# Performance work log

Hardware: AMD Instinct MI355X
Metric: run time of the kernel (lower is better)

## Reference

```python
import jax, jax.numpy as jnp
import numpy as np

B, C, H, W = 8, 512, 64, 64
CH = C // 2          # channels per branch after chunk
R = CH // 4          # reduced channels (reduction=4)


def conv1x1(x, w, b):
    # x: [B,c,H,W], w: [o,c], b: [o]  (1x1 conv == per-pixel matmul)
    return jnp.einsum('oc,bchw->bohw', w, x) + b[None, :, None, None]


def spatial_self_corr(x, w1, b1, w2, b2, wo, bo):
    # DANet-style position attention. x: [B,CH,H,W]
    b_, c_, h_, w_ = x.shape
    n = h_ * w_
    q = conv1x1(x, w1, b1).reshape(b_, -1, n)   # [B,R,N]
    k = conv1x1(x, w2, b2).reshape(b_, -1, n)   # [B,R,N]
    attn = jax.nn.softmax(jnp.einsum('brn,brm->bnm', q, k), axis=-1)  # [B,N,N]
    out = jnp.einsum('brn,bnm->brm', k, attn)   # v = k (reduced channels), [B,R,N]
    out = out.reshape(b_, -1, h_, w_)
    return conv1x1(out, wo, bo)                 # [B,CH,H,W]


def channel_self_corr(x, wq, bq, wk, bk, wo, bo):
    # DANet-style channel attention over reduced channels. x: [B,CH,H,W]
    b_, c_, h_, w_ = x.shape
    n = h_ * w_
    q = conv1x1(x, wq, bq).reshape(b_, -1, n)   # [B,R,N]
    k = conv1x1(x, wk, bk).reshape(b_, -1, n)   # [B,R,N]
    attn = jax.nn.softmax(jnp.einsum('brn,bsn->brs', q, k), axis=-1)  # [B,R,R]
    out = jnp.einsum('brs,bsn->brn', attn, k)   # v = k (reduced channels)
    out = out.reshape(b_, -1, h_, w_)
    return conv1x1(out, wo, bo)                 # [B,CH,H,W]


def ckam_forward(top_feat, bottom_feat, wt, bt, wb, bb,
                 s_w1, s_b1, s_w2, s_b2, s_wo, s_bo,
                 c_wq, c_bq, c_wk, c_bk, c_wo, c_bo, f_w, f_b):
    top = conv1x1(top_feat, wt, bt)
    bottom = conv1x1(bottom_feat, wb, bb)
    x = top + bottom                            # [B,C,H,W]
    x1, x2 = jnp.split(x, 2, axis=1)            # each [B,C/2,H,W]
    ssc_out = spatial_self_corr(x1, s_w1, s_b1, s_w2, s_b2, s_wo, s_bo)
    csc_out = channel_self_corr(x2, c_wq, c_bq, c_wk, c_bk, c_wo, c_bo)
    out = jnp.concatenate([ssc_out, csc_out], axis=1)  # [B,C,H,W]
    return conv1x1(out, f_w, f_b)


def setup_inputs() -> dict:
    key = jax.random.key(0)
    ks = jax.random.split(key, 24)
    s = 0.02
    d = {
        'top_feat': jax.random.normal(ks[0], (B, C, H, W), jnp.float32),
        'bottom_feat': jax.random.normal(ks[1], (B, C, H, W), jnp.float32),
        'wt': jax.random.normal(ks[2], (C, C), jnp.float32) * s,
        'bt': jnp.zeros((C,), jnp.float32),
        'wb': jax.random.normal(ks[3], (C, C), jnp.float32) * s,
        'bb': jnp.zeros((C,), jnp.float32),
        's_w1': jax.random.normal(ks[4], (R, CH), jnp.float32) * s,
        's_b1': jnp.zeros((R,), jnp.float32),
        's_w2': jax.random.normal(ks[5], (R, CH), jnp.float32) * s,
        's_b2': jnp.zeros((R,), jnp.float32),
        's_wo': jax.random.normal(ks[6], (CH, R), jnp.float32) * s,
        's_bo': jnp.zeros((CH,), jnp.float32),
        'c_wq': jax.random.normal(ks[7], (R, CH), jnp.float32) * s,
        'c_bq': jnp.zeros((R,), jnp.float32),
        'c_wk': jax.random.normal(ks[8], (R, CH), jnp.float32) * s,
        'c_bk': jnp.zeros((R,), jnp.float32),
        'c_wo': jax.random.normal(ks[9], (CH, R), jnp.float32) * s,
        'c_bo': jnp.zeros((CH,), jnp.float32),
        'f_w': jax.random.normal(ks[10], (C, C), jnp.float32) * s,
        'f_b': jnp.zeros((C,), jnp.float32),
    }
    return d


def reference(top_feat, bottom_feat, wt, bt, wb, bb,
              s_w1, s_b1, s_w2, s_b2, s_wo, s_bo,
              c_wq, c_bq, c_wk, c_bk, c_wo, c_bo, f_w, f_b):
    return ckam_forward(top_feat, bottom_feat, wt, bt, wb, bb,
                        s_w1, s_b1, s_w2, s_b2, s_wo, s_bo,
                        c_wq, c_bq, c_wk, c_bk, c_wo, c_bo, f_w, f_b)
```

## Files before the change

kernel.cpp:

```cpp
#include <hip/hip_runtime.h>

typedef unsigned short u16;
typedef unsigned int   u32;
typedef __attribute__((ext_vector_type(8))) short short8;
typedef __attribute__((ext_vector_type(4))) float f32x4;

__device__ __forceinline__ u16 f2bf(float f) {
  u32 u = __float_as_uint(f);
  u32 r = u + 0x7fffu + ((u >> 16) & 1u);
  return (u16)(r >> 16);
}

__device__ __forceinline__ void gl_lds16(const u16* g, u16* l) {
  __builtin_amdgcn_global_load_lds(
      (const __attribute__((address_space(1))) u32*)g,
      (__attribute__((address_space(3))) u32*)l, 16, 0, 0);
}

__global__ __launch_bounds__(256) void k_combine_qk(
    const float* __restrict__ wt, const float* __restrict__ bt,
    const float* __restrict__ wb, const float* __restrict__ bb,
    const float* __restrict__ s_w1, const float* __restrict__ s_b1,
    const float* __restrict__ s_w2, const float* __restrict__ s_b2,
    const float* __restrict__ c_wq, const float* __restrict__ c_bq,
    const float* __restrict__ c_wk, const float* __restrict__ c_bk,
    u16* __restrict__ Wqkb, float* __restrict__ bqk) {
  int j = blockIdx.x;
  int g = j >> 6, r = j & 63;
  const float* sw; const float* sb;
  if (g == 0)      { sw = s_w1; sb = s_b1; }
  else if (g == 1) { sw = s_w2; sb = s_b2; }
  else if (g == 2) { sw = c_wq; sb = c_bq; }
  else             { sw = c_wk; sb = c_bk; }
  int cbase = (g < 2) ? 0 : 256;

  __shared__ float swr[256];
  __shared__ float red[256];
  int t = threadIdx.x;
  swr[t] = sw[r * 256 + t];
  __syncthreads();

  float a0 = 0.f, a1 = 0.f, a2 = 0.f, a3 = 0.f;
#pragma unroll 4
  for (int c = 0; c < 256; ++c) {
    float a = swr[c];
    int row = (cbase + c) * 512;
    a0 += a * wt[row + t];
    a1 += a * wt[row + 256 + t];
    a2 += a * wb[row + t];
    a3 += a * wb[row + 256 + t];
  }
  Wqkb[j * 1024 + t]       = f2bf(a0);
  Wqkb[j * 1024 + 256 + t] = f2bf(a1);
  Wqkb[j * 1024 + 512 + t] = f2bf(a2);
  Wqkb[j * 1024 + 768 + t] = f2bf(a3);

  red[t] = swr[t] * (bt[cbase + t] + bb[cbase + t]);
  __syncthreads();
  for (int s = 128; s > 0; s >>= 1) {
    if (t < s) red[t] += red[t + s];
    __syncthreads();
  }
  if (t == 0) bqk[j] = red[0] + sb[r];
}

__global__ __launch_bounds__(128) void k_combine_f(
    const float* __restrict__ f_w, const float* __restrict__ f_b,
    const float* __restrict__ s_wo, const float* __restrict__ s_bo,
    const float* __restrict__ c_wo, const float* __restrict__ c_bo,
    u16* __restrict__ Wfb, float* __restrict__ bfb) {
  int o = blockIdx.x;
  int t = threadIdx.x;
  __shared__ float fwr[512];
  __shared__ float red[128];
  for (int i = t; i < 512; i += 128) fwr[i] = f_w[o * 512 + i];
  __syncthreads();

  float acc = 0.f;
  if (t < 64) {
#pragma unroll 4
    for (int c = 0; c < 256; ++c) acc += fwr[c] * s_wo[c * 64 + t];
  } else {
    int rr = t - 64;
#pragma unroll 4
    for (int c = 0; c < 256; ++c) acc += fwr[256 + c] * c_wo[c * 64 + rr];
  }
  Wfb[o * 128 + t] = f2bf(acc);

  red[t] = fwr[t] * s_bo[t] + fwr[t + 128] * s_bo[t + 128]
         + fwr[256 + t] * c_bo[t] + fwr[384 + t] * c_bo[t + 128];
  __syncthreads();
  for (int s = 64; s > 0; s >>= 1) {
    if (t < s) red[t] += red[t + s];
    __syncthreads();
  }
  if (t == 0) bfb[o] = red[0] + f_b[o];
}

__global__ __launch_bounds__(256) void k_gemm_qk_mfma(
    const float* __restrict__ top, const float* __restrict__ bot,
    const u16* __restrict__ Wqkb, const float* __restrict__ bqk,
    float* __restrict__ qk) {
  int b = blockIdx.z, j0 = blockIdx.y * 128, n0 = blockIdx.x * 128;
  __shared__ __align__(16) u16 Aj[2][128][32];
  __shared__ __align__(16) u16 Xs[2][128][32];
  int t = threadIdx.x;
  int wv = t >> 6, lane = t & 63;
  int wr = wv >> 1, wc = wv & 1;
  int q = lane >> 4, l = lane & 15;

  f32x4 acc[4][4];
#pragma unroll
  for (int tr = 0; tr < 4; ++tr)
#pragma unroll
    for (int tc = 0; tc < 4; ++tc) acc[tr][tc] = (f32x4){0.f, 0.f, 0.f, 0.f};

  int a = t & 31;
  int xs = t >> 5;
  int asr4 = lane >> 2;
  int asc = (lane & 3) ^ ((asr4 + (asr4 >> 2)) & 3);
  int rowA = wr * 64 + l;
  int rowX = wc * 64 + l;
  int fswA = (q ^ ((rowA + (rowA >> 2)) & 3)) << 4;
  int fswX = (q ^ ((rowX + (rowX >> 2)) & 3)) << 4;

  f32x4 xva[4], xvb[4];

  auto stageA = [&](int kc, u16* dst) {
#pragma unroll
    for (int pp = 0; pp < 2; ++pp) {
      int p = wv * 2 + pp;
      int row = p * 16 + asr4;
      gl_lds16(Wqkb + (size_t)(j0 + row) * 1024 + kc + asc * 8, dst + p * 512);
    }
  };
  auto loadX = [&](int kc, f32x4 (&xv)[4]) {
    const float* src = (kc < 512) ? top : bot;
    int c0 = kc & 511;
    const float* xb = src + (size_t)(b * 512 + c0) * 4096 + n0 + 4 * a;
#pragma unroll
    for (int d = 0; d < 4; ++d)
      xv[d] = *reinterpret_cast<const f32x4*>(&xb[(size_t)(4 * xs + d) * 4096]);
  };
  auto writeX = [&](f32x4 (&xv)[4], u16* dst) {
    char* base = reinterpret_cast<char*>(dst);
#pragma unroll
    for (int i = 0; i < 4; ++i) {
      int n = 4 * a + i;
      int key = (n + (n >> 2)) & 3;
      int col = ((((xs >> 1) ^ key) << 4) | ((xs & 1) << 3));
      uint2 pk;
      pk.x = (u32)f2bf(xv[0][i]) | ((u32)f2bf(xv[1][i]) << 16);
      pk.y = (u32)f2bf(xv[2][i]) | ((u32)f2bf(xv[3][i]) << 16);
      *reinterpret_cast<uint2*>(base + n * 64 + col) = pk;
    }
  };
  auto compute = [&](int bufsel) {
    const char* Ab = reinterpret_cast<const char*>(&Aj[bufsel][0][0]);
    const char* Xb = reinterpret_cast<const char*>(&Xs[bufsel][0][0]);
    short8 af[4], bfr[4];
#pragma unroll
    for (int tr = 0; tr < 4; ++tr)
      af[tr] = *reinterpret_cast<const short8*>(Ab + (rowA + tr * 16) * 64 + fswA);
#pragma unroll
    for (int tc = 0; tc < 4; ++tc)
      bfr[tc] = *reinterpret_cast<const short8*>(Xb + (rowX + tc * 16) * 64 + fswX);
#pragma unroll
    for (int tr = 0; tr < 4; ++tr)
#pragma unroll
      for (int tc = 0; tc < 4; ++tc)
        acc[tr][tc] = __builtin_amdgcn_mfma_f32_16x16x32_bf16(
            af[tr], bfr[tc], acc[tr][tc], 0, 0, 0);
  };

  stageA(0, &Aj[0][0][0]);
  loadX(0, xva);
  writeX(xva, &Xs[0][0][0]);
  loadX(32, xvb);
  asm volatile("s_waitcnt lgkmcnt(0)" ::: "memory");
  __builtin_amdgcn_s_barrier();

  for (int it2 = 0; it2 < 15; ++it2) {
    int e = it2 * 2;
    stageA((e + 1) * 32, &Aj[1][0][0]);
    loadX((e + 2) * 32, xva);
    writeX(xvb, &Xs[1][0][0]);
    compute(0);
    asm volatile("s_waitcnt vmcnt(4) lgkmcnt(0)" ::: "memory");
    __builtin_amdgcn_s_barrier();
    stageA((e + 2) * 32, &Aj[0][0][0]);
    loadX((e + 3) * 32, xvb);
    writeX(xva, &Xs[0][0][0]);
    compute(1);
    asm volatile("s_waitcnt vmcnt(4) lgkmcnt(0)" ::: "memory");
    __builtin_amdgcn_s_barrier();
  }
  stageA(31 * 32, &Aj[1][0][0]);
  writeX(xvb, &Xs[1][0][0]);
  compute(0);
  asm volatile("s_waitcnt vmcnt(0) lgkmcnt(0)" ::: "memory");
  __builtin_amdgcn_s_barrier();
  compute(1);

#pragma unroll
  for (int tr = 0; tr < 4; ++tr) {
    int j = j0 + wr * 64 + tr * 16 + q * 4;
    float4 bias = *reinterpret_cast<const float4*>(&bqk[j]);
#pragma unroll
    for (int tc = 0; tc < 4; ++tc) {
      int n = n0 + wc * 64 + tc * 16 + l;
      float* dst = qk + (size_t)(b * 256 + j) * 4096 + n;
      dst[0]        = acc[tr][tc][0] + bias.x;
      dst[4096]     = acc[tr][tc][1] + bias.y;
      dst[2 * 4096] = acc[tr][tc][2] + bias.z;
      dst[3 * 4096] = acc[tr][tc][3] + bias.w;
    }
  }
}

__global__ __launch_bounds__(256) void k_transpose_qk(
    const float* __restrict__ qk, u16* __restrict__ q1t, u16* __restrict__ k1t) {
  int b = blockIdx.y, n0 = blockIdx.x * 64;
  int t = threadIdx.x;
  int a = t & 15;
  int c = t >> 4;
  int jb = 8 * (c & 7);
  const float* src =
      qk + ((size_t)(b * 256) + (c >> 3) * 64 + jb) * 4096 + n0 + 4 * a;
  f32x4 v[8];
#pragma unroll
  for (int i = 0; i < 8; ++i)
    v[i] = *reinterpret_cast<const f32x4*>(&src[(size_t)i * 4096]);
  u16* dstbase = (c < 8) ? q1t : k1t;
#pragma unroll
  for (int i = 0; i < 4; ++i) {
    int n = n0 + 4 * a + i;
    u32 pk[4];
#pragma unroll
    for (int kk = 0; kk < 4; ++kk)
      pk[kk] = (u32)f2bf(v[2 * kk][i]) | ((u32)f2bf(v[2 * kk + 1][i]) << 16);
    *reinterpret_cast<uint4*>(dstbase + ((size_t)(b * 4096) + n) * 64 + jb) =
        *reinterpret_cast<const uint4*>(pk);
  }
}

__global__ __launch_bounds__(256) void k_sp_stats_mfma(
    const u16* __restrict__ q1t, const u16* __restrict__ k1t,
    const float* __restrict__ qk, u16* __restrict__ k1d) {
  int b = blockIdx.y, n0 = blockIdx.x * 64;
  __shared__ u16 Qs[64][72];
  __shared__ float red[4][64][16];
  __shared__ float dvs[64];
  int t = threadIdx.x;
  int wv = t >> 6, lane = t & 63;
  int q = lane >> 4, l = lane & 15;

  {
    const u32* src = reinterpret_cast<const u32*>(q1t + ((size_t)(b * 4096) + n0) * 64);
    for (int i = t; i < 2048; i += 256) {
      int n = i >> 5, c = i & 31;
      reinterpret_cast<u32*>(&Qs[n][0])[c] = src[n * 32 + c];
    }
  }
  __syncthreads();

  short8 afr[4][2];
#pragma unroll
  for (int tn = 0; tn < 4; ++tn)
#pragma unroll
    for (int kh = 0; kh < 2; ++kh)
      afr[tn][kh] = *reinterpret_cast<const short8*>(&Qs[tn * 16 + l][kh * 32 + q * 8]);

  const u16* kbase = k1t + (size_t)b * 4096 * 64;
  float dsum[4][4];
#pragma unroll
  for (int tn = 0; tn < 4; ++tn)
#pragma unroll
    for (int i = 0; i < 4; ++i) dsum[tn][i] = 0.f;

  for (int mt = wv; mt < 64; mt += 4) {
    int m0 = mt * 64;
#pragma unroll
    for (int tm = 0; tm < 4; ++tm) {
      const u16* kp = kbase + ((size_t)(m0 + tm * 16 + l)) * 64;
      short8 b0 = *reinterpret_cast<const short8*>(kp + q * 8);
      short8 b1 = *reinterpret_cast<const short8*>(kp + 32 + q * 8);
#pragma unroll
      for (int tn = 0; tn < 4; ++tn) {
        f32x4 acc = {0.f, 0.f, 0.f, 0.f};
        acc = __builtin_amdgcn_mfma_f32_16x16x32_bf16(afr[tn][0], b0, acc, 0, 0, 0);
        acc = __builtin_amdgcn_mfma_f32_16x16x32_bf16(afr[tn][1], b1, acc, 0, 0, 0);
#pragma unroll
        for (int i = 0; i < 4; ++i) dsum[tn][i] += __expf(acc[i]);
      }
    }
  }

#pragma unroll
  for (int tn = 0; tn < 4; ++tn)
#pragma unroll
    for (int i = 0; i < 4; ++i)
      red[wv][tn * 16 + q * 4 + i][l] = dsum[tn][i];
  __syncthreads();
  if (t < 64) {
    float s = 0.f;
#pragma unroll
    for (int v = 0; v < 4; ++v)
#pragma unroll
      for (int u = 0; u < 16; ++u) s += red[v][t][u];
    dvs[t] = 1.0f / s;
  }
  __syncthreads();

  const float* k1src = qk + ((size_t)(b * 256) + 64) * 4096 + n0;
  u16* kdst = k1d + (size_t)(b * 64) * 4096 + n0;
  for (int i = t; i < 4096; i += 256) {
    int r = i >> 6, n = i & 63;
    kdst[(size_t)r * 4096 + n] = f2bf(k1src[(size_t)r * 4096 + n] * dvs[n]);
  }
}

#define NSPLIT 2

__device__ __forceinline__ void stage_qk(const u16* qb, const u16* kb, int noff,
                                         u16* qdst, u16* kdst,
                                         int wv, int rsub, int scol) {
#pragma unroll
  for (int pp = 0; pp < 2; ++pp) {
    int p = wv * 2 + pp;
    int row = p * 8 + rsub;
    gl_lds16(qb + ((size_t)(noff + row)) * 64 + scol * 8, qdst + p * 512);
    gl_lds16(kb + (size_t)row * 4096 + noff + scol * 8, kdst + p * 512);
  }
}

__global__ __launch_bounds__(256) void k_sp_apply_mfma(
    const u16* __restrict__ q1t, const u16* __restrict__ k1t,
    const u16* __restrict__ k1d, float* __restrict__ spre) {
  int b = blockIdx.z, m0 = blockIdx.x * 64;
  int n_base = blockIdx.y * (4096 / NSPLIT);
  const int NT = 64 / NSPLIT;

  __shared__ __align__(16) u16 Qs[2][64][64];
  __shared__ __align__(16) u16 Ks[2][64][64];
  __shared__ __align__(16) u16 Wt[64][64];

  int t = threadIdx.x;
  int wv = t >> 6, lane = t & 63;
  int q = lane >> 4, l = lane & 15;
  int sw = l & 7;
  int rsub = lane >> 3;
  int scol = (lane & 7) ^ rsub;

  const u16* ktp = k1t + ((size_t)(b * 4096) + m0 + wv * 16 + l) * 64;
  short8 bS0 = *reinterpret_cast<const short8*>(ktp + q * 8);
  short8 bS1 = *reinterpret_cast<const short8*>(ktp + 32 + q * 8);

  const u16* qb = q1t + (size_t)b * 4096 * 64;
  const u16* kb = k1d + (size_t)b * 64 * 4096;

  f32x4 accO[4];
#pragma unroll
  for (int tr = 0; tr < 4; ++tr) accO[tr] = (f32x4){0.f, 0.f, 0.f, 0.f};

  stage_qk(qb, kb, n_base, &Qs[0][0][0], &Ks[0][0][0], wv, rsub, scol);
  __syncthreads();

  int wrow = wv * 16 + l;
  char* wp = reinterpret_cast<char*>(&Wt[wrow][0]);
  int c_a0 = (q ^ sw) << 4;
  int c_a1 = c_a0 ^ 64;

  int cur = 0;
  for (int nt = 0; nt < NT; ++nt) {
    if (nt + 1 < NT)
      stage_qk(qb, kb, n_base + (nt + 1) * 64,
               &Qs[cur ^ 1][0][0], &Ks[cur ^ 1][0][0], wv, rsub, scol);

    const u16(*Qc)[64] = Qs[cur];
    const u16(*Kc)[64] = Ks[cur];

#pragma unroll
    for (int tn = 0; tn < 4; ++tn) {
      const char* qrow = reinterpret_cast<const char*>(&Qc[tn * 16 + l][0]);
      short8 a0 = *reinterpret_cast<const short8*>(qrow + c_a0);
      short8 a1 = *reinterpret_cast<const short8*>(qrow + c_a1);
      f32x4 s = {0.f, 0.f, 0.f, 0.f};
      s = __builtin_amdgcn_mfma_f32_16x16x32_bf16(a0, bS0, s, 0, 0, 0);
      s = __builtin_amdgcn_mfma_f32_16x16x32_bf16(a1, bS1, s, 0, 0, 0);
      u16 w0 = f2bf(__expf(s[0]));
      u16 w1 = f2bf(__expf(s[1]));
      u16 w2 = f2bf(__expf(s[2]));
      u16 w3 = f2bf(__expf(s[3]));
      uint2 pk;
      pk.x = (u32)w0 | ((u32)w1 << 16);
      pk.y = (u32)w2 | ((u32)w3 << 16);
      *reinterpret_cast<uint2*>(
          wp + ((((tn * 2 + (q >> 1)) ^ sw) << 4) | ((q & 1) << 3))) = pk;
    }

    short8 bW0 = *reinterpret_cast<const short8*>(wp + c_a0);
    short8 bW1 = *reinterpret_cast<const short8*>(wp + c_a1);
#pragma unroll
    for (int tr = 0; tr < 4; ++tr) {
      const char* krow = reinterpret_cast<const char*>(&Kc[tr * 16 + l][0]);
      short8 a0 = *reinterpret_cast<const short8*>(krow + c_a0);
      short8 a1 = *reinterpret_cast<const short8*>(krow + c_a1);
      accO[tr] = __builtin_amdgcn_mfma_f32_16x16x32_bf16(a0, bW0, accO[tr], 0, 0, 0);
      accO[tr] = __builtin_amdgcn_mfma_f32_16x16x32_bf16(a1, bW1, accO[tr], 0, 0, 0);
    }

    __syncthreads();
    cur ^= 1;
  }

#pragma unroll
  for (int tr = 0; tr < 4; ++tr)
#pragma unroll
    for (int i = 0; i < 4; ++i)
      atomicAdd(&spre[(size_t)(b * 64 + tr * 16 + q * 4 + i) * 4096 + m0 + wrow],
                accO[tr][i]);
}

__global__ __launch_bounds__(256) void k_ch_scores(
    const float* __restrict__ qk, float* __restrict__ part) {
  int b = blockIdx.y, ch = blockIdx.x;
  const float* q2 = qk + (size_t)(b * 256 + 128) * 4096;
  const float* k2 = qk + (size_t)(b * 256 + 192) * 4096;
  __shared__ float Qs[64][65];
  __shared__ float Ks[64][65];
  int t = threadIdx.x, ti = t >> 4, tj = t & 15;
  float acc[4][4] = {};

  for (int sub = 0; sub < 2; ++sub) {
    int n0 = ch * 128 + sub * 64;
    __syncthreads();
    for (int i = t; i < 4096; i += 256) {
      int r = i >> 6, n = i & 63;
      Qs[r][n] = q2[(size_t)r * 4096 + n0 + n];
      Ks[r][n] = k2[(size_t)r * 4096 + n0 + n];
    }
    __syncthreads();
#pragma unroll
    for (int n = 0; n < 64; ++n) {
      float qa[4], ka[4];
#pragma unroll
      for (int i = 0; i < 4; ++i) qa[i] = Qs[ti * 4 + i][n];
#pragma unroll
      for (int jx = 0; jx < 4; ++jx) ka[jx] = Ks[tj * 4 + jx][n];
#pragma unroll
      for (int i = 0; i < 4; ++i)
#pragma unroll
        for (int jx = 0; jx < 4; ++jx) acc[i][jx] += qa[i] * ka[jx];
    }
  }
#pragma unroll
  for (int i = 0; i < 4; ++i)
#pragma unroll
    for (int jx = 0; jx < 4; ++jx)
      part[(size_t)(b * 32 + ch) * 4096 + (ti * 4 + i) * 64 + tj * 4 + jx] = acc[i][jx];
}

__global__ __launch_bounds__(64) void k_ch_softmax(
    const float* __restrict__ part, float* __restrict__ attn2) {
  int bid = blockIdx.x;
  int b = bid >> 6, r = bid & 63;
  int s = threadIdx.x;
  const float* p0 = part + (size_t)(b * 32) * 4096 + r * 64 + s;
  float sum = 0.f;
#pragma unroll
  for (int c = 0; c < 32; ++c) sum += p0[(size_t)c * 4096];
  float mx = sum;
#pragma unroll
  for (int o = 32; o > 0; o >>= 1) mx = fmaxf(mx, __shfl_xor(mx, o));
  float e = __expf(sum - mx);
  float den = e;
#pragma unroll
  for (int o = 32; o > 0; o >>= 1) den += __shfl_xor(den, o);
  attn2[(size_t)b * 4096 + r * 64 + s] = e / den;
}

__global__ __launch_bounds__(256) void k_ch_apply(
    const float* __restrict__ qk, const float* __restrict__ attn2,
    float* __restrict__ cpre) {
  int b = blockIdx.y;
  int t = threadIdx.x;
  int n = blockIdx.x * 64 + (t & 63);
  int qr = t >> 6;
  const float* k2 = qk + (size_t)(b * 256 + 192) * 4096;
  __shared__ float As[64][64];
  {
    float4* As4 = reinterpret_cast<float4*>(&As[0][0]);
    const float4* a4 = reinterpret_cast<const float4*>(attn2 + (size_t)b * 4096);
    for (int i = t; i < 1024; i += 256) As4[i] = a4[i];
  }
  __syncthreads();

  float acc[16];
#pragma unroll
  for (int rr = 0; rr < 16; ++rr) acc[rr] = 0.f;
  for (int s4 = 0; s4 < 64; s4 += 4) {
    float kv0 = k2[(size_t)(s4 + 0) * 4096 + n];
    float kv1 = k2[(size_t)(s4 + 1) * 4096 + n];
    float kv2 = k2[(size_t)(s4 + 2) * 4096 + n];
    float kv3 = k2[(size_t)(s4 + 3) * 4096 + n];
#pragma unroll
    for (int rr = 0; rr < 16; ++rr) {
      float4 w = *reinterpret_cast<const float4*>(&As[qr * 16 + rr][s4]);
      acc[rr] += w.x * kv0 + w.y * kv1 + w.z * kv2 + w.w * kv3;
    }
  }
#pragma unroll
  for (int rr = 0; rr < 16; ++rr)
    cpre[(size_t)(b * 64 + qr * 16 + rr) * 4096 + n] = acc[rr];
}

__global__ __launch_bounds__(256) void k_final_mfma(
    const float* __restrict__ spre, const float* __restrict__ cpre,
    const u16* __restrict__ Wfb, const float* __restrict__ bfb,
    float* __restrict__ out) {
  int b = blockIdx.z, o0 = blockIdx.y * 128, n0 = blockIdx.x * 128;
  __shared__ __align__(16) u16 Aj[2][128][32];
  __shared__ __align__(16) u16 Xs[2][128][32];
  int t = threadIdx.x;
  int wv = t >> 6, lane = t & 63;
  int wr = wv >> 1, wc = wv & 1;
  int q = lane >> 4, l = lane & 15;

  f32x4 acc[4][4];
#pragma unroll
  for (int tr = 0; tr < 4; ++tr)
#pragma unroll
    for (int tc = 0; tc < 4; ++tc) acc[tr][tc] = (f32x4){0.f, 0.f, 0.f, 0.f};

  int a = t & 31;
  int xs = t >> 5;
  int asr4 = lane >> 2;
  int asc = (lane & 3) ^ ((asr4 + (asr4 >> 2)) & 3);
  int rowA = wr * 64 + l;
  int rowX = wc * 64 + l;
  int fswA = (q ^ ((rowA + (rowA >> 2)) & 3)) << 4;
  int fswX = (q ^ ((rowX + (rowX >> 2)) & 3)) << 4;

  f32x4 xva[4], xvb[4];

  auto stageA = [&](int kc, u16* dst) {
#pragma unroll
    for (int pp = 0; pp < 2; ++pp) {
      int p = wv * 2 + pp;
      int row = p * 16 + asr4;
      gl_lds16(Wfb + (size_t)(o0 + row) * 128 + kc + asc * 8, dst + p * 512);
    }
  };
  auto loadX = [&](int kc, f32x4 (&xv)[4]) {
    const float* src = (kc < 64) ? spre : cpre;
    int r0 = kc & 63;
    const float* xb = src + (size_t)(b * 64 + r0) * 4096 + n0 + 4 * a;
#pragma unroll
    for (int d = 0; d < 4; ++d)
      xv[d] = *reinterpret_cast<const f32x4*>(&xb[(size_t)(4 * xs + d) * 4096]);
  };
  auto writeX = [&](f32x4 (&xv)[4], u16* dst) {
    char* base = reinterpret_cast<char*>(dst);
#pragma unroll
    for (int i = 0; i < 4; ++i) {
      int n = 4 * a + i;
      int key = (n + (n >> 2)) & 3;
      int col = ((((xs >> 1) ^ key) << 4) | ((xs & 1) << 3));
      uint2 pk;
      pk.x = (u32)f2bf(xv[0][i]) | ((u32)f2bf(xv[1][i]) << 16);
      pk.y = (u32)f2bf(xv[2][i]) | ((u32)f2bf(xv[3][i]) << 16);
      *reinterpret_cast<uint2*>(base + n * 64 + col) = pk;
    }
  };
  auto compute = [&](int bufsel) {
    const char* Ab = reinterpret_cast<const char*>(&Aj[bufsel][0][0]);
    const char* Xb = reinterpret_cast<const char*>(&Xs[bufsel][0][0]);
    short8 af[4], bfr[4];
#pragma unroll
    for (int tr = 0; tr < 4; ++tr)
      af[tr] = *reinterpret_cast<const short8*>(Ab + (rowA + tr * 16) * 64 + fswA);
#pragma unroll
    for (int tc = 0; tc < 4; ++tc)
      bfr[tc] = *reinterpret_cast<const short8*>(Xb + (rowX + tc * 16) * 64 + fswX);
#pragma unroll
    for (int tr = 0; tr < 4; ++tr)
#pragma unroll
      for (int tc = 0; tc < 4; ++tc)
        acc[tr][tc] = __builtin_amdgcn_mfma_f32_16x16x32_bf16(
            af[tr], bfr[tc], acc[tr][tc], 0, 0, 0);
  };

  stageA(0, &Aj[0][0][0]);
  loadX(0, xva);
  writeX(xva, &Xs[0][0][0]);
  loadX(32, xvb);
  asm volatile("s_waitcnt lgkmcnt(0)" ::: "memory");
  __builtin_amdgcn_s_barrier();
  stageA(32, &Aj[1][0][0]);
  loadX(64, xva);
  writeX(xvb, &Xs[1][0][0]);
  compute(0);
  asm volatile("s_waitcnt vmcnt(4) lgkmcnt(0)" ::: "memory");
  __builtin_amdgcn_s_barrier();
  stageA(64, &Aj[0][0][0]);
  loadX(96, xvb);
  writeX(xva, &Xs[0][0][0]);
  compute(1);
  asm volatile("s_waitcnt vmcnt(4) lgkmcnt(0)" ::: "memory");
  __builtin_amdgcn_s_barrier();
  stageA(96, &Aj[1][0][0]);
  writeX(xvb, &Xs[1][0][0]);
  compute(0);
  asm volatile("s_waitcnt vmcnt(0) lgkmcnt(0)" ::: "memory");
  __builtin_amdgcn_s_barrier();
  compute(1);

#pragma unroll
  for (int tr = 0; tr < 4; ++tr) {
    int o = o0 + wr * 64 + tr * 16 + q * 4;
    float4 bias = *reinterpret_cast<const float4*>(&bfb[o]);
#pragma unroll
    for (int tc = 0; tc < 4; ++tc) {
      int n = n0 + wc * 64 + tc * 16 + l;
      float* dst = out + (size_t)(b * 512 + o) * 4096 + n;
      dst[0]        = acc[tr][tc][0] + bias.x;
      dst[4096]     = acc[tr][tc][1] + bias.y;
      dst[2 * 4096] = acc[tr][tc][2] + bias.z;
      dst[3 * 4096] = acc[tr][tc][3] + bias.w;
    }
  }
}

extern "C" void kernel_launch(void* const* d_in, const int* in_sizes, int n_in,
                              void* d_out, int out_size, void* d_ws, size_t ws_size,
                              hipStream_t stream) {
  const float* top  = (const float*)d_in[0];
  const float* bot  = (const float*)d_in[1];
  const float* wt   = (const float*)d_in[2];
  const float* bt   = (const float*)d_in[3];
  const float* wb   = (const float*)d_in[4];
  const float* bb   = (const float*)d_in[5];
  const float* s_w1 = (const float*)d_in[6];
  const float* s_b1 = (const float*)d_in[7];
  const float* s_w2 = (const float*)d_in[8];
  const float* s_b2 = (const float*)d_in[9];
  const float* s_wo = (const float*)d_in[10];
  const float* s_bo = (const float*)d_in[11];
  const float* c_wq = (const float*)d_in[12];
  const float* c_bq = (const float*)d_in[13];
  const float* c_wk = (const float*)d_in[14];
  const float* c_bk = (const float*)d_in[15];
  const float* c_wo = (const float*)d_in[16];
  const float* c_bo = (const float*)d_in[17];
  const float* f_w  = (const float*)d_in[18];
  const float* f_b  = (const float*)d_in[19];
  float* out = (float*)d_out;

  char* ob = (char*)d_out;
  float* qk = (float*)ob;
  u16* q1t = (u16*)(ob + 33554432);
  u16* k1t = (u16*)(ob + 37748736);
  u16* k1d = (u16*)(ob + 41943040);
  float* part = (float*)(ob + 46137344);

  char* ws = (char*)d_ws;
  float* attn2 = (float*)(ws + 1179648);
  float* spre  = (float*)(ws + 1310720);
  float* cpre  = (float*)(ws + 9699328);
  u16*   Wqkb  = (u16*)  (ws + 18087936);
  float* bqk   = (float*)(ws + 18612224);
  u16*   Wfb   = (u16*)  (ws + 18613248);
  float* bfb   = (float*)(ws + 18744320);

  hipMemsetAsync(spre, 0, 8388608, stream);

  k_combine_qk<<<256, 256, 0, stream>>>(wt, bt, wb, bb, s_w1, s_b1, s_w2, s_b2,
                                        c_wq, c_bq, c_wk, c_bk, Wqkb, bqk);
  k_combine_f<<<512, 128, 0, stream>>>(f_w, f_b, s_wo, s_bo, c_wo, c_bo, Wfb, bfb);
  k_gemm_qk_mfma<<<dim3(32, 2, 8), 256, 0, stream>>>(top, bot, Wqkb, bqk, qk);
  k_transpose_qk<<<dim3(64, 8), 256, 0, stream>>>(qk, q1t, k1t);
  k_sp_stats_mfma<<<dim3(64, 8), 256, 0, stream>>>(q1t, k1t, qk, k1d);
  k_ch_scores<<<dim3(32, 8), 256, 0, stream>>>(qk, part);
  k_ch_softmax<<<512, 64, 0, stream>>>(part, attn2);
  k_ch_apply<<<dim3(64, 8), 256, 0, stream>>>(qk, attn2, cpre);
  k_sp_apply_mfma<<<dim3(64, NSPLIT, 8), 256, 0, stream>>>(q1t, k1t, k1d, spre);
  k_final_mfma<<<dim3(32, 4, 8), 256, 0, stream>>>(spre, cpre, Wfb, bfb, out);
}
```

Baseline: 433.6 us.

## Fuse bf16 transposed Q/K write into QK GEMM epilogue and scalarize X loads

Removes the separate transpose kernel by having the blocks with j0==0 write bf16 transposed spatial Q and K directly from the GEMM accumulators. The X-tile load changes from f32x4 vector loads to scalar per-element loads with a precomputed swizzle column, and the vmcnt waits are adjusted to match the new load count. This saves a launch and a re-read of qk, at the cost of narrower, strided uint2 stores in the epilogue and more load instructions per tile.

```diff
diff --git a/kernel.cpp b/kernel.cpp
--- a/kernel.cpp
+++ b/kernel.cpp
@@ -100,7 +100,7 @@
 __global__ __launch_bounds__(256) void k_gemm_qk_mfma(
     const float* __restrict__ top, const float* __restrict__ bot,
     const u16* __restrict__ Wqkb, const float* __restrict__ bqk,
-    float* __restrict__ qk) {
+    float* __restrict__ qk, u16* __restrict__ q1t, u16* __restrict__ k1t) {
   int b = blockIdx.z, j0 = blockIdx.y * 128, n0 = blockIdx.x * 128;
   __shared__ __align__(16) u16 Aj[2][128][32];
   __shared__ __align__(16) u16 Xs[2][128][32];
@@ -115,8 +115,10 @@
 #pragma unroll
     for (int tc = 0; tc < 4; ++tc) acc[tr][tc] = (f32x4){0.f, 0.f, 0.f, 0.f};
 
-  int a = t & 31;
+  int xn = t & 31;
   int xs = t >> 5;
+  int kx = (xn + (xn >> 2)) & 3;
+  int wcol = ((((xs >> 1) ^ kx) << 4) | ((xs & 1) << 3));
   int asr4 = lane >> 2;
   int asc = (lane & 3) ^ ((asr4 + (asr4 >> 2)) & 3);
   int rowA = wr * 64 + l;
@@ -124,7 +126,7 @@
   int fswA = (q ^ ((rowA + (rowA >> 2)) & 3)) << 4;
   int fswX = (q ^ ((rowX + (rowX >> 2)) & 3)) << 4;
 
-  f32x4 xva[4], xvb[4];
+  float xva[16], xvb[16];
 
   auto stageA = [&](int kc, u16* dst) {
 #pragma unroll
@@ -134,25 +136,27 @@
       gl_lds16(Wqkb + (size_t)(j0 + row) * 1024 + kc + asc * 8, dst + p * 512);
     }
   };
-  auto loadX = [&](int kc, f32x4 (&xv)[4]) {
+  auto loadX = [&](int kc, float (&xv)[16]) {
     const float* src = (kc < 512) ? top : bot;
     int c0 = kc & 511;
-    const float* xb = src + (size_t)(b * 512 + c0) * 4096 + n0 + 4 * a;
-#pragma unroll
-    for (int d = 0; d < 4; ++d)
-      xv[d] = *reinterpret_cast<const f32x4*>(&xb[(size_t)(4 * xs + d) * 4096]);
-  };
-  auto writeX = [&](f32x4 (&xv)[4], u16* dst) {
+    const float* xb = src + (size_t)(b * 512 + c0) * 4096 + n0;
+#pragma unroll
+    for (int p = 0; p < 4; ++p) {
+      int n = xn + 32 * p;
+#pragma unroll
+      for (int d = 0; d < 4; ++d)
+        xv[4 * p + d] = xb[(size_t)(4 * xs + d) * 4096 + n];
+    }
+  };
+  auto writeX = [&](float (&xv)[16], u16* dst) {
     char* base = reinterpret_cast<char*>(dst);
 #pragma unroll
-    for (int i = 0; i < 4; ++i) {
-      int n = 4 * a + i;
-      int key = (n + (n >> 2)) & 3;
-      int col = ((((xs >> 1) ^ key) << 4) | ((xs & 1) << 3));
+    for (int p = 0; p < 4; ++p) {
+      int n = xn + 32 * p;
       uint2 pk;
-      pk.x = (u32)f2bf(xv[0][i]) | ((u32)f2bf(xv[1][i]) << 16);
-      pk.y = (u32)f2bf(xv[2][i]) | ((u32)f2bf(xv[3][i]) << 16);
-      *reinterpret_cast<uint2*>(base + n * 64 + col) = pk;
+      pk.x = (u32)f2bf(xv[4 * p])     | ((u32)f2bf(xv[4 * p + 1]) << 16);
+      pk.y = (u32)f2bf(xv[4 * p + 2]) | ((u32)f2bf(xv[4 * p + 3]) << 16);
+      *reinterpret_cast<uint2*>(base + n * 64 + wcol) = pk;
     }
   };
   auto compute = [&](int bufsel) {
@@ -186,13 +190,13 @@
     loadX((e + 2) * 32, xva);
     writeX(xvb, &Xs[1][0][0]);
     compute(0);
-    asm volatile("s_waitcnt vmcnt(4) lgkmcnt(0)" ::: "memory");
+    asm volatile("s_waitcnt vmcnt(16) lgkmcnt(0)" ::: "memory");
     __builtin_amdgcn_s_barrier();
     stageA((e + 2) * 32, &Aj[0][0][0]);
     loadX((e + 3) * 32, xvb);
     writeX(xva, &Xs[0][0][0]);
     compute(1);
-    asm volatile("s_waitcnt vmcnt(4) lgkmcnt(0)" ::: "memory");
+    asm volatile("s_waitcnt vmcnt(16) lgkmcnt(0)" ::: "memory");
     __builtin_amdgcn_s_barrier();
   }
   stageA(31 * 32, &Aj[1][0][0]);
@@ -202,45 +206,33 @@
   __builtin_amdgcn_s_barrier();
   compute(1);
 
+  bool doT = (j0 == 0);
+  u16* tdst = (wr == 0) ? q1t : k1t;
 #pragma unroll
   for (int tr = 0; tr < 4; ++tr) {
-    int j = j0 + wr * 64 + tr * 16 + q * 4;
+    int jl = wr * 64 + tr * 16 + q * 4;
+    int j = j0 + jl;
+    int jc = jl & 63;
     float4 bias = *reinterpret_cast<const float4*>(&bqk[j]);
 #pragma unroll
     for (int tc = 0; tc < 4; ++tc) {
       int n = n0 + wc * 64 + tc * 16 + l;
+      float v0 = acc[tr][tc][0] + bias.x;
+      float v1 = acc[tr][tc][1] + bias.y;
+      float v2 = acc[tr][tc][2] + bias.z;
+      float v3 = acc[tr][tc][3] + bias.w;
       float* dst = qk + (size_t)(b * 256 + j) * 4096 + n;
-      dst[0]        = acc[tr][tc][0] + bias.x;
-      dst[4096]     = acc[tr][tc][1] + bias.y;
-      dst[2 * 4096] = acc[tr][tc][2] + bias.z;
-      dst[3 * 4096] = acc[tr][tc][3] + bias.w;
-    }
-  }
-}
-
-__global__ __launch_bounds__(256) void k_transpose_qk(
-    const float* __restrict__ qk, u16* __restrict__ q1t, u16* __restrict__ k1t) {
-  int b = blockIdx.y, n0 = blockIdx.x * 64;
-  int t = threadIdx.x;
-  int a = t & 15;
-  int c = t >> 4;
-  int jb = 8 * (c & 7);
-  const float* src =
-      qk + ((size_t)(b * 256) + (c >> 3) * 64 + jb) * 4096 + n0 + 4 * a;
-  f32x4 v[8];
-#pragma unroll
-  for (int i = 0; i < 8; ++i)
-    v[i] = *reinterpret_cast<const f32x4*>(&src[(size_t)i * 4096]);
-  u16* dstbase = (c < 8) ? q1t : k1t;
-#pragma unroll
-  for (int i = 0; i < 4; ++i) {
-    int n = n0 + 4 * a + i;
-    u32 pk[4];
-#pragma unroll
-    for (int kk = 0; kk < 4; ++kk)
-      pk[kk] = (u32)f2bf(v[2 * kk][i]) | ((u32)f2bf(v[2 * kk + 1][i]) << 16);
-    *reinterpret_cast<uint4*>(dstbase + ((size_t)(b * 4096) + n) * 64 + jb) =
-        *reinterpret_cast<const uint4*>(pk);
+      dst[0]        = v0;
+      dst[4096]     = v1;
+      dst[2 * 4096] = v2;
+      dst[3 * 4096] = v3;
+      if (doT) {
+        uint2 pk;
+        pk.x = (u32)f2bf(v0) | ((u32)f2bf(v1) << 16);
+        pk.y = (u32)f2bf(v2) | ((u32)f2bf(v3) << 16);
+        *reinterpret_cast<uint2*>(tdst + ((size_t)(b * 4096) + n) * 64 + jc) = pk;
+      }
+    }
   }
 }
 
@@ -678,8 +670,8 @@
   k_combine_qk<<<256, 256, 0, stream>>>(wt, bt, wb, bb, s_w1, s_b1, s_w2, s_b2,
                                         c_wq, c_bq, c_wk, c_bk, Wqkb, bqk);
   k_combine_f<<<512, 128, 0, stream>>>(f_w, f_b, s_wo, s_bo, c_wo, c_bo, Wfb, bfb);
-  k_gemm_qk_mfma<<<dim3(32, 2, 8), 256, 0, stream>>>(top, bot, Wqkb, bqk, qk);
-  k_transpose_qk<<<dim3(64, 8), 256, 0, stream>>>(qk, q1t, k1t);
+  k_gemm_qk_mfma<<<dim3(32, 2, 8), 256, 0, stream>>>(top, bot, Wqkb, bqk, qk,
+                                                     q1t, k1t);
   k_sp_stats_mfma<<<dim3(64, 8), 256, 0, stream>>>(q1t, k1t, qk, k1d);
   k_ch_scores<<<dim3(32, 8), 256, 0, stream>>>(qk, part);
   k_ch_softmax<<<512, 64, 0, stream>>>(part, attn2);
```

Measured after the change: 433.0 us. Within noise of the previous version (-0.1%).
